# Performance work log

Hardware: AMD Instinct MI355X
Metric: run time of the kernel (lower is better)

The kernel has to match this reference:

```python
import jax, jax.numpy as jnp
import numpy as np

NUM_HEADS = 8

def setup_inputs() -> dict:
    key = jax.random.key(0)
    qkv = jax.random.normal(key, (8, 1536, 2048), dtype=jnp.float32)
    return {"qkv": qkv}

def reference(qkv) -> jnp.ndarray:
    bs, width, length = qkv.shape
    ch = width // (3 * NUM_HEADS)
    qkv_r = qkv.reshape(bs * NUM_HEADS, 3 * ch, length)
    q, k, v = jnp.split(qkv_r, 3, axis=1)  # each [bs*H, ch, length]
    scale = 1.0 / jnp.sqrt(jnp.sqrt(jnp.float32(ch)))
    # scores [bs*H, t, s]
    weight = jnp.einsum('bct,bcs->bts', q * scale, k * scale)
    weight = jax.nn.softmax(weight.astype(jnp.float32), axis=-1).astype(qkv.dtype)
    a = jnp.einsum('bts,bcs->bct', weight, v)  # [bs*H, ch, length]
    return a.reshape(bs, -1, length)
```

## Files before the change

### kernel.cpp

```cpp
#include <hip/hip_runtime.h>
#include <hip/hip_fp16.h>


typedef _Float16 half8 __attribute__((ext_vector_type(8)));
typedef _Float16 half4 __attribute__((ext_vector_type(4)));
typedef float floatx4 __attribute__((ext_vector_type(4)));

__global__ __launch_bounds__(256, 4) void attn_kernel(const float* __restrict__ qkv,
                                                      float* __restrict__ out)
{
    __shared__ _Float16 Kt[64 * 64];
    __shared__ _Float16 Vt[64 * 64];
    __shared__ _Float16 Pt[128 * 64];

    const int tid  = threadIdx.x;
    const int wave = tid >> 6;
    const int lane = tid & 63;
    const int llo  = lane & 15;
    const int lhi  = lane >> 4;

    const int blk  = blockIdx.x;
    const int slot = blk >> 3;
    const int bh   = (blk & 7) * 8 + (slot >> 4);
    const int tile = slot & 15;
    const int t0   = tile * 128;

    const float* qb = qkv + (size_t)bh * 393216;
    const float* kb = qb + 131072;
    const float* vb = qb + 262144;

    const float C  = 0.125f * 1.44269504088896f;
    const float B2 = 6.0f;

    half8 qf[2][2];
    const int twbase = t0 + wave * 32;
    #pragma unroll
    for (int nt = 0; nt < 2; ++nt) {
        const int t = twbase + nt * 16 + llo;
        #pragma unroll
        for (int ck = 0; ck < 2; ++ck)
            #pragma unroll
            for (int j = 0; j < 8; ++j) {
                const int c = ck * 32 + lhi * 8 + j;
                qf[nt][ck][j] = (_Float16)(qb[c * 2048 + t] * C);
            }
    }

    const int kc4 = (tid >> 4) * 4;
    const int ksq = (tid & 15) * 4;
    const int vc  = tid >> 4;
    const int vs  = (tid & 15) * 4;

    int kwoff[4];
    #pragma unroll
    for (int sr = 0; sr < 4; ++sr) {
        const int s  = ksq + sr;
        const int sw = ((s >> 2) ^ s) & 7;
        kwoff[sr] = s * 64 + ((((kc4 >> 3) ^ sw) & 7) << 3) + (kc4 & 7);
    }
    int vwoff[4];
    #pragma unroll
    for (int i = 0; i < 4; ++i) {
        const int c = vc + 16 * i;
        vwoff[i] = c * 64 + ((((vs >> 3) ^ (c & 7)) & 7) << 3) + (vs & 7);
    }
    int kroff[4][2];
    #pragma unroll
    for (int ms = 0; ms < 4; ++ms) {
        const int s  = ms * 16 + llo;
        const int sw = ((s >> 2) ^ s) & 7;
        kroff[ms][0] = s * 64 + (((lhi ^ sw) & 7) << 3);
        kroff[ms][1] = s * 64 + ((((lhi + 4) ^ sw) & 7) << 3);
    }
    int pwoff[2][4];
    #pragma unroll
    for (int nt = 0; nt < 2; ++nt) {
        const int row = wave * 32 + nt * 16 + llo;
        #pragma unroll
        for (int ms = 0; ms < 4; ++ms)
            pwoff[nt][ms] = row * 64 + ((((2 * ms + (lhi >> 1)) ^ (llo & 7)) & 7) << 3)
                          + 4 * (lhi & 1);
    }
    int proff[2][2];
    #pragma unroll
    for (int nt = 0; nt < 2; ++nt) {
        const int row = wave * 32 + nt * 16 + llo;
        #pragma unroll
        for (int sk = 0; sk < 2; ++sk)
            proff[nt][sk] = row * 64 + ((((sk * 4 + lhi) ^ (llo & 7)) & 7) << 3);
    }
    int vroff[4][2];
    #pragma unroll
    for (int mc = 0; mc < 4; ++mc) {
        const int row = mc * 16 + llo;
        #pragma unroll
        for (int sk = 0; sk < 2; ++sk)
            vroff[mc][sk] = row * 64 + ((((sk * 4 + lhi) ^ (llo & 7)) & 7) << 3);
    }

    floatx4 kr[4], vr[4];
    auto loadKV = [&](int s0) {
        #pragma unroll
        for (int r = 0; r < 4; ++r)
            kr[r] = *reinterpret_cast<const floatx4*>(kb + (kc4 + r) * 2048 + s0 + ksq);
        #pragma unroll
        for (int i = 0; i < 4; ++i)
            vr[i] = *reinterpret_cast<const floatx4*>(vb + (vc + 16 * i) * 2048 + s0 + vs);
    };
    auto storeKV = [&]() {
        #pragma unroll
        for (int sr = 0; sr < 4; ++sr) {
            half4 h = { (_Float16)kr[0][sr], (_Float16)kr[1][sr],
                        (_Float16)kr[2][sr], (_Float16)kr[3][sr] };
            *reinterpret_cast<half4*>(&Kt[kwoff[sr]]) = h;
        }
        #pragma unroll
        for (int i = 0; i < 4; ++i) {
            half4 h = { (_Float16)vr[i][0], (_Float16)vr[i][1],
                        (_Float16)vr[i][2], (_Float16)vr[i][3] };
            *reinterpret_cast<half4*>(&Vt[vwoff[i]]) = h;
        }
    };

    floatx4 O[2][4];
    #pragma unroll
    for (int nt = 0; nt < 2; ++nt)
        #pragma unroll
        for (int mc = 0; mc < 4; ++mc)
            O[nt][mc] = (floatx4){0.f, 0.f, 0.f, 0.f};
    float l_run[2] = {0.f, 0.f};

    loadKV(0);

    for (int it = 0; it < 32; ++it) {
        __syncthreads();
        storeKV();
        __syncthreads();
        if (it + 1 < 32) loadKV((it + 1) * 64);

        #pragma unroll
        for (int ms = 0; ms < 4; ++ms) {
            half8 a0 = *reinterpret_cast<const half8*>(&Kt[kroff[ms][0]]);
            half8 a1 = *reinterpret_cast<const half8*>(&Kt[kroff[ms][1]]);
            #pragma unroll
            for (int nt = 0; nt < 2; ++nt) {
                floatx4 acc = (floatx4){-B2, -B2, -B2, -B2};
                acc = __builtin_amdgcn_mfma_f32_16x16x32_f16(a0, qf[nt][0], acc, 0, 0, 0);
                acc = __builtin_amdgcn_mfma_f32_16x16x32_f16(a1, qf[nt][1], acc, 0, 0, 0);
                half4 ph;
                float l = 0.f;
                #pragma unroll
                for (int r = 0; r < 4; ++r) {
                    const float p = __builtin_amdgcn_exp2f(acc[r]);
                    l += p;
                    ph[r] = (_Float16)p;
                }
                l_run[nt] += l;
                *reinterpret_cast<half4*>(&Pt[pwoff[nt][ms]]) = ph;
            }
        }

        #pragma unroll
        for (int sk = 0; sk < 2; ++sk) {
            half8 bp[2];
            #pragma unroll
            for (int nt = 0; nt < 2; ++nt)
                bp[nt] = *reinterpret_cast<const half8*>(&Pt[proff[nt][sk]]);
            #pragma unroll
            for (int mc = 0; mc < 4; ++mc) {
                half8 av = *reinterpret_cast<const half8*>(&Vt[vroff[mc][sk]]);
                #pragma unroll
                for (int nt = 0; nt < 2; ++nt)
                    O[nt][mc] = __builtin_amdgcn_mfma_f32_16x16x32_f16(av, bp[nt], O[nt][mc], 0, 0, 0);
            }
        }
    }

    float* ob = out + (size_t)bh * 131072;
    #pragma unroll
    for (int nt = 0; nt < 2; ++nt) {
        float l = l_run[nt];
        l += __shfl_xor(l, 16, 64);
        l += __shfl_xor(l, 32, 64);
        const float inv = 1.0f / l;
        const int t = twbase + nt * 16 + llo;
        #pragma unroll
        for (int mc = 0; mc < 4; ++mc)
            #pragma unroll
            for (int r = 0; r < 4; ++r) {
                const int c = mc * 16 + lhi * 4 + r;
                ob[c * 2048 + t] = O[nt][mc][r] * inv;
            }
    }
}

extern "C" void kernel_launch(void* const* d_in, const int* in_sizes, int n_in,
                              void* d_out, int out_size, void* d_ws, size_t ws_size,
                              hipStream_t stream) {
    const float* qkv = (const float*)d_in[0];
    float* out = (float*)d_out;
    attn_kernel<<<dim3(1024), dim3(256), 0, stream>>>(qkv, out);
}
```

Before: 222.2 us.

## Double-buffer K/V in LDS with register prefetch and split P tile

Adds A/B LDS buffers for K and V plus two register staging sets. The kernel now prefetches two tiles ahead and stores the next tile to LDS while computing on the current one, which halves the barriers per iteration. The P scratch is halved by processing the scores in two 32-column phases, each followed immediately by its PV MFMAs. s_setprio hints are added around the MFMA groups. The extra registers and LDS may lower occupancy, and the P buffer is reused within each iteration without a barrier because every wave reads only its own rows.

```diff
diff --git a/kernel.cpp b/kernel.cpp
--- a/kernel.cpp
+++ b/kernel.cpp
@@ -9,9 +9,11 @@
 __global__ __launch_bounds__(256, 4) void attn_kernel(const float* __restrict__ qkv,
                                                       float* __restrict__ out)
 {
-    __shared__ _Float16 Kt[64 * 64];
-    __shared__ _Float16 Vt[64 * 64];
-    __shared__ _Float16 Pt[128 * 64];
+    __shared__ _Float16 KtA[64 * 64];
+    __shared__ _Float16 VtA[64 * 64];
+    __shared__ _Float16 KtB[64 * 64];
+    __shared__ _Float16 VtB[64 * 64];
+    __shared__ _Float16 Pt[128 * 32];
 
     const int tid  = threadIdx.x;
     const int wave = tid >> 6;
@@ -32,24 +34,38 @@
     const float C  = 0.125f * 1.44269504088896f;
     const float B2 = 6.0f;
 
-    half8 qf[2][2];
-    const int twbase = t0 + wave * 32;
-    #pragma unroll
-    for (int nt = 0; nt < 2; ++nt) {
-        const int t = twbase + nt * 16 + llo;
-        #pragma unroll
-        for (int ck = 0; ck < 2; ++ck)
-            #pragma unroll
-            for (int j = 0; j < 8; ++j) {
-                const int c = ck * 32 + lhi * 8 + j;
-                qf[nt][ck][j] = (_Float16)(qb[c * 2048 + t] * C);
-            }
-    }
-
     const int kc4 = (tid >> 4) * 4;
     const int ksq = (tid & 15) * 4;
     const int vc  = tid >> 4;
     const int vs  = (tid & 15) * 4;
+
+    floatx4 krA[4], vrA[4], krB[4], vrB[4];
+
+    auto loadKV = [&](floatx4 (&kr)[4], floatx4 (&vr)[4], int s0) {
+        #pragma unroll
+        for (int r = 0; r < 4; ++r)
+            kr[r] = *reinterpret_cast<const floatx4*>(kb + (kc4 + r) * 2048 + s0 + ksq);
+        #pragma unroll
+        for (int i = 0; i < 4; ++i)
+            vr[i] = *reinterpret_cast<const floatx4*>(vb + (vc + 16 * i) * 2048 + s0 + vs);
+    };
+
+    loadKV(krA, vrA, 0);
+    loadKV(krB, vrB, 64);
+
+    half8 qf[2][2];
+    const int twbase = t0 + wave * 32;
+    #pragma unroll
+    for (int nt = 0; nt < 2; ++nt) {
+        const int t = twbase + nt * 16 + llo;
+        #pragma unroll
+        for (int ck = 0; ck < 2; ++ck)
+            #pragma unroll
+            for (int j = 0; j < 8; ++j) {
+                const int c = ck * 32 + lhi * 8 + j;
+                qf[nt][ck][j] = (_Float16)(qb[c * 2048 + t] * C);
+            }
+    }
 
     int kwoff[4];
     #pragma unroll
@@ -72,22 +88,21 @@
         kroff[ms][0] = s * 64 + (((lhi ^ sw) & 7) << 3);
         kroff[ms][1] = s * 64 + ((((lhi + 4) ^ sw) & 7) << 3);
     }
-    int pwoff[2][4];
+    int pwoff[2][2];
     #pragma unroll
     for (int nt = 0; nt < 2; ++nt) {
         const int row = wave * 32 + nt * 16 + llo;
-        #pragma unroll
-        for (int ms = 0; ms < 4; ++ms)
-            pwoff[nt][ms] = row * 64 + ((((2 * ms + (lhi >> 1)) ^ (llo & 7)) & 7) << 3)
-                          + 4 * (lhi & 1);
-    }
-    int proff[2][2];
+        const int swz = (llo >> 1) & 3;
+        #pragma unroll
+        for (int ms2 = 0; ms2 < 2; ++ms2)
+            pwoff[nt][ms2] = row * 32 + ((((2 * ms2 + (lhi >> 1)) ^ swz) & 3) << 3)
+                           + 4 * (lhi & 1);
+    }
+    int proff[2];
     #pragma unroll
     for (int nt = 0; nt < 2; ++nt) {
         const int row = wave * 32 + nt * 16 + llo;
-        #pragma unroll
-        for (int sk = 0; sk < 2; ++sk)
-            proff[nt][sk] = row * 64 + ((((sk * 4 + lhi) ^ (llo & 7)) & 7) << 3);
+        proff[nt] = row * 32 + (((lhi ^ ((llo >> 1) & 3)) & 3) << 3);
     }
     int vroff[4][2];
     #pragma unroll
@@ -98,16 +113,8 @@
             vroff[mc][sk] = row * 64 + ((((sk * 4 + lhi) ^ (llo & 7)) & 7) << 3);
     }
 
-    floatx4 kr[4], vr[4];
-    auto loadKV = [&](int s0) {
-        #pragma unroll
-        for (int r = 0; r < 4; ++r)
-            kr[r] = *reinterpret_cast<const floatx4*>(kb + (kc4 + r) * 2048 + s0 + ksq);
-        #pragma unroll
-        for (int i = 0; i < 4; ++i)
-            vr[i] = *reinterpret_cast<const floatx4*>(vb + (vc + 16 * i) * 2048 + s0 + vs);
-    };
-    auto storeKV = [&]() {
+    auto storeKV = [&](_Float16* Kt, _Float16* Vt,
+                       const floatx4 (&kr)[4], const floatx4 (&vr)[4]) {
         #pragma unroll
         for (int sr = 0; sr < 4; ++sr) {
             half4 h = { (_Float16)kr[0][sr], (_Float16)kr[1][sr],
@@ -130,50 +137,63 @@
             O[nt][mc] = (floatx4){0.f, 0.f, 0.f, 0.f};
     float l_run[2] = {0.f, 0.f};
 
-    loadKV(0);
-
-    for (int it = 0; it < 32; ++it) {
-        __syncthreads();
-        storeKV();
-        __syncthreads();
-        if (it + 1 < 32) loadKV((it + 1) * 64);
-
-        #pragma unroll
-        for (int ms = 0; ms < 4; ++ms) {
-            half8 a0 = *reinterpret_cast<const half8*>(&Kt[kroff[ms][0]]);
-            half8 a1 = *reinterpret_cast<const half8*>(&Kt[kroff[ms][1]]);
-            #pragma unroll
-            for (int nt = 0; nt < 2; ++nt) {
-                floatx4 acc = (floatx4){-B2, -B2, -B2, -B2};
-                acc = __builtin_amdgcn_mfma_f32_16x16x32_f16(a0, qf[nt][0], acc, 0, 0, 0);
-                acc = __builtin_amdgcn_mfma_f32_16x16x32_f16(a1, qf[nt][1], acc, 0, 0, 0);
-                half4 ph;
-                float l = 0.f;
+    auto compute = [&](const _Float16* K, const _Float16* V) {
+        #pragma unroll
+        for (int ph = 0; ph < 2; ++ph) {
+            #pragma unroll
+            for (int ms2 = 0; ms2 < 2; ++ms2) {
+                const int ms = ph * 2 + ms2;
+                half8 a0 = *reinterpret_cast<const half8*>(&K[kroff[ms][0]]);
+                half8 a1 = *reinterpret_cast<const half8*>(&K[kroff[ms][1]]);
                 #pragma unroll
-                for (int r = 0; r < 4; ++r) {
-                    const float p = __builtin_amdgcn_exp2f(acc[r]);
-                    l += p;
-                    ph[r] = (_Float16)p;
+                for (int nt = 0; nt < 2; ++nt) {
+                    floatx4 acc = (floatx4){-B2, -B2, -B2, -B2};
+                    __builtin_amdgcn_s_setprio(1);
+                    acc = __builtin_amdgcn_mfma_f32_16x16x32_f16(a0, qf[nt][0], acc, 0, 0, 0);
+                    acc = __builtin_amdgcn_mfma_f32_16x16x32_f16(a1, qf[nt][1], acc, 0, 0, 0);
+                    __builtin_amdgcn_s_setprio(0);
+                    half4 phv;
+                    float l = 0.f;
+                    #pragma unroll
+                    for (int r = 0; r < 4; ++r) {
+                        const float p = __builtin_amdgcn_exp2f(acc[r]);
+                        l += p;
+                        phv[r] = (_Float16)p;
+                    }
+                    l_run[nt] += l;
+                    *reinterpret_cast<half4*>(&Pt[pwoff[nt][ms2]]) = phv;
                 }
-                l_run[nt] += l;
-                *reinterpret_cast<half4*>(&Pt[pwoff[nt][ms]]) = ph;
-            }
+            }
+            half8 bp0 = *reinterpret_cast<const half8*>(&Pt[proff[0]]);
+            half8 bp1 = *reinterpret_cast<const half8*>(&Pt[proff[1]]);
+            __builtin_amdgcn_s_setprio(1);
+            #pragma unroll
+            for (int mc = 0; mc < 4; ++mc) {
+                half8 av = *reinterpret_cast<const half8*>(&V[vroff[mc][ph]]);
+                O[0][mc] = __builtin_amdgcn_mfma_f32_16x16x32_f16(av, bp0, O[0][mc], 0, 0, 0);
+                O[1][mc] = __builtin_amdgcn_mfma_f32_16x16x32_f16(av, bp1, O[1][mc], 0, 0, 0);
+            }
+            __builtin_amdgcn_s_setprio(0);
         }
-
-        #pragma unroll
-        for (int sk = 0; sk < 2; ++sk) {
-            half8 bp[2];
-            #pragma unroll
-            for (int nt = 0; nt < 2; ++nt)
-                bp[nt] = *reinterpret_cast<const half8*>(&Pt[proff[nt][sk]]);
-            #pragma unroll
-            for (int mc = 0; mc < 4; ++mc) {
-                half8 av = *reinterpret_cast<const half8*>(&Vt[vroff[mc][sk]]);
-                #pragma unroll
-                for (int nt = 0; nt < 2; ++nt)
-                    O[nt][mc] = __builtin_amdgcn_mfma_f32_16x16x32_f16(av, bp[nt], O[nt][mc], 0, 0, 0);
-            }
-        }
+    };
+
+    storeKV(KtA, VtA, krA, vrA);
+    asm volatile("s_waitcnt lgkmcnt(0)" ::: "memory");
+    __builtin_amdgcn_s_barrier();
+
+    #pragma unroll 1
+    for (int it = 0; it < 32; it += 2) {
+        if (it + 2 < 32) loadKV(krA, vrA, (it + 2) * 64);
+        storeKV(KtB, VtB, krB, vrB);
+        compute(KtA, VtA);
+        asm volatile("s_waitcnt lgkmcnt(0)" ::: "memory");
+        __builtin_amdgcn_s_barrier();
+
+        if (it + 3 < 32) loadKV(krB, vrB, (it + 3) * 64);
+        if (it + 2 < 32) storeKV(KtA, VtA, krA, vrA);
+        compute(KtB, VtB);
+        asm volatile("s_waitcnt lgkmcnt(0)" ::: "memory");
+        __builtin_amdgcn_s_barrier();
     }
 
     float* ob = out + (size_t)bh * 131072;
```

Result: slower. 595.4 us (+168.0%).
